# Performance work log

Measured on AMD Instinct MI355X. Metric: run time of the kernel, lower is better.

The kernel has to match this reference:

```python
import jax, jax.numpy as jnp
import numpy as np

B, T, D = 256, 512, 256

def setup_inputs() -> dict:
    key = jax.random.key(0)
    k1, k2, k3, k4 = jax.random.split(key, 4)
    ip = jax.random.normal(k1, (B, T, D), dtype=jnp.float32)
    W = jax.random.normal(k2, (D, D), dtype=jnp.float32) * (1.0 / np.sqrt(D))
    b = jax.random.normal(k3, (D,), dtype=jnp.float32) * 0.05
    context = jax.random.normal(k4, (D, 1), dtype=jnp.float32) * 0.05
    return {"ip": ip, "W": W, "b": b, "context": context}

def reference(ip, W, b, context) -> jnp.ndarray:
    # linear -> tanh: [B, T, D]
    h = jnp.tanh(jnp.einsum("btd,ed->bte", ip, W) + b)
    # attention scores over words: [B, T]
    scores = jnp.einsum("btd,d->bt", h, context[:, 0])
    attn = jax.nn.softmax(scores, axis=1)
    # weighted sum over words -> sentence embeddings: [B, D]
    sent_embeds = jnp.einsum("bt,btd->bd", attn, ip)
    return sent_embeds
```

## Files before the change

kernel.cpp:

```cpp
#include <hip/hip_runtime.h>
#include <hip/hip_bf16.h>

#define NBATCH 256
#define NT 512
#define ND 256
#define NROWS (NBATCH * NT)
#define NCHUNK (NROWS / 64)

typedef __attribute__((ext_vector_type(8))) short short8;
typedef __attribute__((ext_vector_type(4))) float floatx4;

__device__ __forceinline__ unsigned short f2bf(float x) {
    unsigned int u = __float_as_uint(x);
    u += 0x7FFFu + ((u >> 16) & 1u);
    return (unsigned short)(u >> 16);
}

__global__ void __launch_bounds__(256) prep_kernel(
    const float* __restrict__ W, unsigned short* __restrict__ wf)
{
    int g  = blockIdx.x * 256 + threadIdx.x;
    int m  = g & 15, q = (g >> 4) & 3, s = (g >> 6) & 7, nb = g >> 9;
    const float* src = W + (nb * 16 + m) * ND + q * 8 + s * 32;
    float4 f0 = *(const float4*)src;
    float4 f1 = *(const float4*)(src + 4);
    short8 v;
    v[0] = (short)f2bf(f0.x); v[1] = (short)f2bf(f0.y);
    v[2] = (short)f2bf(f0.z); v[3] = (short)f2bf(f0.w);
    v[4] = (short)f2bf(f1.x); v[5] = (short)f2bf(f1.y);
    v[6] = (short)f2bf(f1.z); v[7] = (short)f2bf(f1.w);
    *(short8*)(wf + (long)g * 8) = v;
}

__global__ void __launch_bounds__(256, 4) fused_kernel(
    const float* __restrict__ ip,
    const unsigned short* __restrict__ wf,
    const float* __restrict__ bias,
    const float* __restrict__ ctx,
    float* __restrict__ gpart,
    float2* __restrict__ ml)
{
    __shared__ __align__(16) char wsm[32768];
    __shared__ float score_s[64];
    __shared__ float w_s[64];
    short8* lds16 = (short8*)wsm;

    const int tid  = threadIdx.x;
    const int lane = tid & 63;
    const int wv   = tid >> 6;
    const int m    = lane & 15;
    const int q    = lane >> 4;
    const long row0 = (long)blockIdx.x * 64 + wv * 16;

    short8 a[8];
    {
        const float* ar = ip + (row0 + m) * ND + q * 8;
        float4 raw[8];
#pragma unroll
        for (int g = 0; g < 2; ++g) {
#pragma unroll
            for (int i = 0; i < 4; ++i) {
                raw[2 * i]     = *(const float4*)(ar + (4 * g + i) * 32);
                raw[2 * i + 1] = *(const float4*)(ar + (4 * g + i) * 32 + 4);
            }
#pragma unroll
            for (int i = 0; i < 4; ++i) {
                short8 v;
                v[0] = (short)f2bf(raw[2 * i].x); v[1] = (short)f2bf(raw[2 * i].y);
                v[2] = (short)f2bf(raw[2 * i].z); v[3] = (short)f2bf(raw[2 * i].w);
                v[4] = (short)f2bf(raw[2 * i + 1].x); v[5] = (short)f2bf(raw[2 * i + 1].y);
                v[6] = (short)f2bf(raw[2 * i + 1].z); v[7] = (short)f2bf(raw[2 * i + 1].w);
                a[4 * g + i] = v;
            }
        }
    }

    float sc[4] = {0.f, 0.f, 0.f, 0.f};
    const short8* wchunks = (const short8*)wf;

#pragma unroll 1
    for (int stage = 0; stage < 4; ++stage) {
        if (stage) __syncthreads();
#pragma unroll
        for (int u = 0; u < 8; ++u) {
            int c = u * 256 + tid;
            lds16[c] = wchunks[stage * 2048 + c];
        }
        __syncthreads();

#pragma unroll 1
        for (int nbl = 0; nbl < 4; ++nbl) {
            const int e = (stage * 4 + nbl) * 16 + m;
            const short8* wp = lds16 + nbl * 512 + lane;
            short8 w[8];
#pragma unroll
            for (int s = 0; s < 8; ++s) w[s] = wp[s * 64];
            floatx4 acc = {0.f, 0.f, 0.f, 0.f};
#pragma unroll
            for (int s = 0; s < 8; ++s)
                acc = __builtin_amdgcn_mfma_f32_16x16x32_bf16(a[s], w[s], acc, 0, 0, 0);
            const float be  = bias[e];
            const float ce  = ctx[e];
            const float ce2 = ce + ce;
#pragma unroll
            for (int r = 0; r < 4; ++r) {
                float x = acc[r] + be;
                float t = __builtin_amdgcn_rcpf(__expf(x + x) + 1.f);
                sc[r] = __builtin_fmaf(-ce2, t, sc[r] + ce);
            }
        }
    }

#pragma unroll
    for (int off = 8; off >= 1; off >>= 1) {
#pragma unroll
        for (int r = 0; r < 4; ++r)
            sc[r] += __shfl_xor(sc[r], off, 64);
    }
    if (m == 0) {
#pragma unroll
        for (int r = 0; r < 4; ++r)
            score_s[wv * 16 + q * 4 + r] = sc[r];
    }
    __syncthreads();

    float s = score_s[lane];
    float mx = s;
#pragma unroll
    for (int off = 32; off >= 1; off >>= 1) mx = fmaxf(mx, __shfl_xor(mx, off, 64));
    float w = __expf(s - mx);
    float lsum = w;
#pragma unroll
    for (int off = 32; off >= 1; off >>= 1) lsum += __shfl_xor(lsum, off, 64);
    if (wv == 0) w_s[lane] = w;
    if (tid == 0) ml[blockIdx.x] = make_float2(mx, lsum);
    __syncthreads();

    const float4* base = (const float4*)ip + ((long)blockIdx.x * 64 + wv * 16) * 64 + lane;
    float4 acc4 = {0.f, 0.f, 0.f, 0.f};
#pragma unroll
    for (int r = 0; r < 16; ++r) {
        float wt = w_s[wv * 16 + r];
        float4 v = base[(long)r * 64];
        acc4.x += wt * v.x; acc4.y += wt * v.y;
        acc4.z += wt * v.z; acc4.w += wt * v.w;
    }
    float4* part4 = (float4*)wsm;
    part4[wv * 64 + lane] = acc4;
    __syncthreads();
    if (tid < 64) {
        float4 r0 = part4[tid],       r1 = part4[64 + tid];
        float4 r2 = part4[128 + tid], r3 = part4[192 + tid];
        float4 o;
        o.x = r0.x + r1.x + r2.x + r3.x;
        o.y = r0.y + r1.y + r2.y + r3.y;
        o.z = r0.z + r1.z + r2.z + r3.z;
        o.w = r0.w + r1.w + r2.w + r3.w;
        ((float4*)gpart)[(long)blockIdx.x * 64 + tid] = o;
    }
}

__global__ void __launch_bounds__(256) combine_kernel(
    const float4* __restrict__ gpart4,
    const float2* __restrict__ ml,
    float4* __restrict__ out4)
{
    const int b = blockIdx.x * 4 + (threadIdx.x >> 6);
    const int c = threadIdx.x & 63;
    const float2* mlb = ml + b * 8;
    float mk[8], lk[8];
#pragma unroll
    for (int k = 0; k < 8; ++k) { float2 p = mlb[k]; mk[k] = p.x; lk[k] = p.y; }
    float M = mk[0];
#pragma unroll
    for (int k = 1; k < 8; ++k) M = fmaxf(M, mk[k]);
    float L = 0.f, f[8];
#pragma unroll
    for (int k = 0; k < 8; ++k) { f[k] = __expf(mk[k] - M); L += f[k] * lk[k]; }
    float4 acc = {0.f, 0.f, 0.f, 0.f};
#pragma unroll
    for (int k = 0; k < 8; ++k) {
        float4 v = gpart4[(long)(b * 8 + k) * 64 + c];
        acc.x += f[k] * v.x; acc.y += f[k] * v.y;
        acc.z += f[k] * v.z; acc.w += f[k] * v.w;
    }
    float inv = 1.f / L;
    acc.x *= inv; acc.y *= inv; acc.z *= inv; acc.w *= inv;
    out4[(long)b * 64 + c] = acc;
}

extern "C" void kernel_launch(void* const* d_in, const int* in_sizes, int n_in,
                              void* d_out, int out_size, void* d_ws, size_t ws_size,
                              hipStream_t stream) {
    const float* ip   = (const float*)d_in[0];
    const float* W    = (const float*)d_in[1];
    const float* bias = (const float*)d_in[2];
    const float* ctx  = (const float*)d_in[3];

    unsigned short* wf = (unsigned short*)d_ws;
    float* gpart = (float*)((char*)d_ws + ND * ND * sizeof(unsigned short));
    float2* ml   = (float2*)((char*)gpart + (long)NCHUNK * ND * sizeof(float));

    prep_kernel<<<32, 256, 0, stream>>>(W, wf);
    fused_kernel<<<NCHUNK, 256, 0, stream>>>(ip, wf, bias, ctx, gpart, ml);
    combine_kernel<<<NBATCH / 4, 256, 0, stream>>>((const float4*)gpart, ml, (float4*)d_out);
}
```

Before: 221.1 us.

## Double rows per block and stream bf16 W from global instead of LDS

Each wave now handles 32 rows (two 16-row MFMA tiles) instead of 16, so every W fragment loaded feeds two MFMAs and the number of blocks halves. The LDS staging of W and its stage barriers are removed; W fragments are read directly from global/L2 per column block. The combine kernel now merges 4 partials per batch instead of 8. This costs more VGPRs (two A-fragment sets, two accumulators) at launch_bounds(256,4), and W global loads no longer go through shared memory.

Result: slower. 238.3 us (+7.8%).

```diff
diff --git a/kernel.cpp b/kernel.cpp
--- a/kernel.cpp
+++ b/kernel.cpp
@@ -5,7 +5,8 @@
 #define NT 512
 #define ND 256
 #define NROWS (NBATCH * NT)
-#define NCHUNK (NROWS / 64)
+#define CHUNK 128
+#define NCHUNK (NROWS / CHUNK)
 
 typedef __attribute__((ext_vector_type(8))) short short8;
 typedef __attribute__((ext_vector_type(4))) float floatx4;
@@ -14,6 +15,15 @@
     unsigned int u = __float_as_uint(x);
     u += 0x7FFFu + ((u >> 16) & 1u);
     return (unsigned short)(u >> 16);
+}
+
+__device__ __forceinline__ short8 cvt8(float4 lo, float4 hi) {
+    short8 v;
+    v[0] = (short)f2bf(lo.x); v[1] = (short)f2bf(lo.y);
+    v[2] = (short)f2bf(lo.z); v[3] = (short)f2bf(lo.w);
+    v[4] = (short)f2bf(hi.x); v[5] = (short)f2bf(hi.y);
+    v[6] = (short)f2bf(hi.z); v[7] = (short)f2bf(hi.w);
+    return v;
 }
 
 __global__ void __launch_bounds__(256) prep_kernel(
@@ -24,12 +34,7 @@
     const float* src = W + (nb * 16 + m) * ND + q * 8 + s * 32;
     float4 f0 = *(const float4*)src;
     float4 f1 = *(const float4*)(src + 4);
-    short8 v;
-    v[0] = (short)f2bf(f0.x); v[1] = (short)f2bf(f0.y);
-    v[2] = (short)f2bf(f0.z); v[3] = (short)f2bf(f0.w);
-    v[4] = (short)f2bf(f1.x); v[5] = (short)f2bf(f1.y);
-    v[6] = (short)f2bf(f1.z); v[7] = (short)f2bf(f1.w);
-    *(short8*)(wf + (long)g * 8) = v;
+    *(short8*)(wf + (long)g * 8) = cvt8(f0, f1);
 }
 
 __global__ void __launch_bounds__(256, 4) fused_kernel(
@@ -40,19 +45,18 @@
     float* __restrict__ gpart,
     float2* __restrict__ ml)
 {
-    __shared__ __align__(16) char wsm[32768];
-    __shared__ float score_s[64];
-    __shared__ float w_s[64];
-    short8* lds16 = (short8*)wsm;
+    __shared__ float score_s[CHUNK];
+    __shared__ float w_s[CHUNK];
+    __shared__ __align__(16) float partial[4][ND];
 
     const int tid  = threadIdx.x;
     const int lane = tid & 63;
     const int wv   = tid >> 6;
     const int m    = lane & 15;
     const int q    = lane >> 4;
-    const long row0 = (long)blockIdx.x * 64 + wv * 16;
-
-    short8 a[8];
+    const long row0 = (long)blockIdx.x * CHUNK + wv * 32;
+
+    short8 a0[8], a1[8];
     {
         const float* ar = ip + (row0 + m) * ND + q * 8;
         float4 raw[8];
@@ -64,99 +68,106 @@
                 raw[2 * i + 1] = *(const float4*)(ar + (4 * g + i) * 32 + 4);
             }
 #pragma unroll
+            for (int i = 0; i < 4; ++i)
+                a0[4 * g + i] = cvt8(raw[2 * i], raw[2 * i + 1]);
+        }
+        const float* br = ar + 16 * ND;
+#pragma unroll
+        for (int g = 0; g < 2; ++g) {
+#pragma unroll
             for (int i = 0; i < 4; ++i) {
-                short8 v;
-                v[0] = (short)f2bf(raw[2 * i].x); v[1] = (short)f2bf(raw[2 * i].y);
-                v[2] = (short)f2bf(raw[2 * i].z); v[3] = (short)f2bf(raw[2 * i].w);
-                v[4] = (short)f2bf(raw[2 * i + 1].x); v[5] = (short)f2bf(raw[2 * i + 1].y);
-                v[6] = (short)f2bf(raw[2 * i + 1].z); v[7] = (short)f2bf(raw[2 * i + 1].w);
-                a[4 * g + i] = v;
+                raw[2 * i]     = *(const float4*)(br + (4 * g + i) * 32);
+                raw[2 * i + 1] = *(const float4*)(br + (4 * g + i) * 32 + 4);
             }
-        }
-    }
-
-    float sc[4] = {0.f, 0.f, 0.f, 0.f};
-    const short8* wchunks = (const short8*)wf;
+#pragma unroll
+            for (int i = 0; i < 4; ++i)
+                a1[4 * g + i] = cvt8(raw[2 * i], raw[2 * i + 1]);
+        }
+    }
+
+    float sc0[4] = {0.f, 0.f, 0.f, 0.f};
+    float sc1[4] = {0.f, 0.f, 0.f, 0.f};
+    const short8* wch = (const short8*)wf;
 
 #pragma unroll 1
-    for (int stage = 0; stage < 4; ++stage) {
-        if (stage) __syncthreads();
-#pragma unroll
-        for (int u = 0; u < 8; ++u) {
-            int c = u * 256 + tid;
-            lds16[c] = wchunks[stage * 2048 + c];
-        }
-        __syncthreads();
-
-#pragma unroll 1
-        for (int nbl = 0; nbl < 4; ++nbl) {
-            const int e = (stage * 4 + nbl) * 16 + m;
-            const short8* wp = lds16 + nbl * 512 + lane;
-            short8 w[8];
-#pragma unroll
-            for (int s = 0; s < 8; ++s) w[s] = wp[s * 64];
-            floatx4 acc = {0.f, 0.f, 0.f, 0.f};
-#pragma unroll
-            for (int s = 0; s < 8; ++s)
-                acc = __builtin_amdgcn_mfma_f32_16x16x32_bf16(a[s], w[s], acc, 0, 0, 0);
-            const float be  = bias[e];
-            const float ce  = ctx[e];
-            const float ce2 = ce + ce;
-#pragma unroll
-            for (int r = 0; r < 4; ++r) {
-                float x = acc[r] + be;
-                float t = __builtin_amdgcn_rcpf(__expf(x + x) + 1.f);
-                sc[r] = __builtin_fmaf(-ce2, t, sc[r] + ce);
-            }
+    for (int nb = 0; nb < 16; ++nb) {
+        const short8* wp = wch + nb * 512 + lane;
+        short8 w[4];
+        floatx4 acc0 = {0.f, 0.f, 0.f, 0.f};
+        floatx4 acc1 = {0.f, 0.f, 0.f, 0.f};
+#pragma unroll
+        for (int s = 0; s < 4; ++s) w[s] = wp[s * 64];
+#pragma unroll
+        for (int s = 0; s < 4; ++s) {
+            acc0 = __builtin_amdgcn_mfma_f32_16x16x32_bf16(a0[s], w[s], acc0, 0, 0, 0);
+            acc1 = __builtin_amdgcn_mfma_f32_16x16x32_bf16(a1[s], w[s], acc1, 0, 0, 0);
+        }
+#pragma unroll
+        for (int s = 0; s < 4; ++s) w[s] = wp[(s + 4) * 64];
+#pragma unroll
+        for (int s = 0; s < 4; ++s) {
+            acc0 = __builtin_amdgcn_mfma_f32_16x16x32_bf16(a0[s + 4], w[s], acc0, 0, 0, 0);
+            acc1 = __builtin_amdgcn_mfma_f32_16x16x32_bf16(a1[s + 4], w[s], acc1, 0, 0, 0);
+        }
+        const int e = nb * 16 + m;
+        const float be  = bias[e];
+        const float ce  = ctx[e];
+        const float ce2 = ce + ce;
+#pragma unroll
+        for (int r = 0; r < 4; ++r) {
+            float x0 = acc0[r] + be;
+            float t0 = __builtin_amdgcn_rcpf(__expf(x0 + x0) + 1.f);
+            sc0[r] = __builtin_fmaf(-ce2, t0, sc0[r] + ce);
+            float x1 = acc1[r] + be;
+            float t1 = __builtin_amdgcn_rcpf(__expf(x1 + x1) + 1.f);
+            sc1[r] = __builtin_fmaf(-ce2, t1, sc1[r] + ce);
         }
     }
 
 #pragma unroll
     for (int off = 8; off >= 1; off >>= 1) {
 #pragma unroll
-        for (int r = 0; r < 4; ++r)
-            sc[r] += __shfl_xor(sc[r], off, 64);
+        for (int r = 0; r < 4; ++r) {
+            sc0[r] += __shfl_xor(sc0[r], off, 64);
+            sc1[r] += __shfl_xor(sc1[r], off, 64);
+        }
     }
     if (m == 0) {
 #pragma unroll
-        for (int r = 0; r < 4; ++r)
-            score_s[wv * 16 + q * 4 + r] = sc[r];
+        for (int r = 0; r < 4; ++r) {
+            score_s[wv * 32 + q * 4 + r]      = sc0[r];
+            score_s[wv * 32 + 16 + q * 4 + r] = sc1[r];
+        }
     }
     __syncthreads();
 
-    float s = score_s[lane];
-    float mx = s;
+    float s0 = score_s[lane], s1 = score_s[64 + lane];
+    float mx = fmaxf(s0, s1);
 #pragma unroll
     for (int off = 32; off >= 1; off >>= 1) mx = fmaxf(mx, __shfl_xor(mx, off, 64));
-    float w = __expf(s - mx);
-    float lsum = w;
-#pragma unroll
-    for (int off = 32; off >= 1; off >>= 1) lsum += __shfl_xor(lsum, off, 64);
-    if (wv == 0) w_s[lane] = w;
-    if (tid == 0) ml[blockIdx.x] = make_float2(mx, lsum);
+    float e0v = __expf(s0 - mx), e1v = __expf(s1 - mx);
+    float ls = e0v + e1v;
+#pragma unroll
+    for (int off = 32; off >= 1; off >>= 1) ls += __shfl_xor(ls, off, 64);
+    if (wv == 0) { w_s[lane] = e0v; w_s[64 + lane] = e1v; }
+    if (tid == 0) ml[blockIdx.x] = make_float2(mx, ls);
     __syncthreads();
 
-    const float4* base = (const float4*)ip + ((long)blockIdx.x * 64 + wv * 16) * 64 + lane;
+    const float4* base = (const float4*)(ip + row0 * ND) + lane;
     float4 acc4 = {0.f, 0.f, 0.f, 0.f};
-#pragma unroll
-    for (int r = 0; r < 16; ++r) {
-        float wt = w_s[wv * 16 + r];
-        float4 v = base[(long)r * 64];
+#pragma unroll 8
+    for (int r = 0; r < 32; ++r) {
+        const float wt = w_s[wv * 32 + r];
+        const float4 v = base[(long)r * 64];
         acc4.x += wt * v.x; acc4.y += wt * v.y;
         acc4.z += wt * v.z; acc4.w += wt * v.w;
     }
-    float4* part4 = (float4*)wsm;
-    part4[wv * 64 + lane] = acc4;
+    ((float4*)&partial[wv][0])[lane] = acc4;
     __syncthreads();
-    if (tid < 64) {
-        float4 r0 = part4[tid],       r1 = part4[64 + tid];
-        float4 r2 = part4[128 + tid], r3 = part4[192 + tid];
-        float4 o;
-        o.x = r0.x + r1.x + r2.x + r3.x;
-        o.y = r0.y + r1.y + r2.y + r3.y;
-        o.z = r0.z + r1.z + r2.z + r3.z;
-        o.w = r0.w + r1.w + r2.w + r3.w;
-        ((float4*)gpart)[(long)blockIdx.x * 64 + tid] = o;
+    {
+        float r = partial[0][tid] + partial[1][tid]
+                + partial[2][tid] + partial[3][tid];
+        gpart[(long)blockIdx.x * ND + tid] = r;
     }
 }
 
@@ -167,20 +178,18 @@
 {
     const int b = blockIdx.x * 4 + (threadIdx.x >> 6);
     const int c = threadIdx.x & 63;
-    const float2* mlb = ml + b * 8;
-    float mk[8], lk[8];
-#pragma unroll
-    for (int k = 0; k < 8; ++k) { float2 p = mlb[k]; mk[k] = p.x; lk[k] = p.y; }
-    float M = mk[0];
-#pragma unroll
-    for (int k = 1; k < 8; ++k) M = fmaxf(M, mk[k]);
-    float L = 0.f, f[8];
-#pragma unroll
-    for (int k = 0; k < 8; ++k) { f[k] = __expf(mk[k] - M); L += f[k] * lk[k]; }
+    const float2* mlb = ml + b * 4;
+    float mk[4], lk[4];
+#pragma unroll
+    for (int k = 0; k < 4; ++k) { float2 p = mlb[k]; mk[k] = p.x; lk[k] = p.y; }
+    float M = fmaxf(fmaxf(mk[0], mk[1]), fmaxf(mk[2], mk[3]));
+    float L = 0.f, f[4];
+#pragma unroll
+    for (int k = 0; k < 4; ++k) { f[k] = __expf(mk[k] - M); L += f[k] * lk[k]; }
     float4 acc = {0.f, 0.f, 0.f, 0.f};
 #pragma unroll
-    for (int k = 0; k < 8; ++k) {
-        float4 v = gpart4[(long)(b * 8 + k) * 64 + c];
+    for (int k = 0; k < 4; ++k) {
+        float4 v = gpart4[(long)(b * 4 + k) * 64 + c];
         acc.x += f[k] * v.x; acc.y += f[k] * v.y;
         acc.z += f[k] * v.z; acc.w += f[k] * v.w;
     }
```
